# Performance work log

Measured on AMD Instinct MI355X. Metric: run time of the kernel, lower is better.

Reference implementation:

```python
import jax, jax.numpy as jnp
from jax import lax
import numpy as np

RNN = 512; FC = 512; COND = 128; FEAT = 80; NCLS = 256; HALF = RNN // 2
PAD = 2; SCALES = (5, 5, 11); MEL_T = 86  # -> 22550 output samples


def setup_inputs() -> dict:
    key = jax.random.key(0)
    ks = jax.random.split(key, 12)
    s = 0.05
    p = {"mels": jax.random.normal(ks[0], (1, FEAT, MEL_T), jnp.float32)}
    ch = FEAT
    for i, sc in enumerate(SCALES):
        k = 2 * sc + 1
        p[f"up_w{i}"] = jax.random.normal(ks[1 + i], (COND, ch, k), jnp.float32) * s
        p[f"up_b{i}"] = jnp.zeros((COND,), jnp.float32)
        ch = COND
    p["Wx"] = jax.random.normal(ks[4], (3 * RNN, 3 + COND), jnp.float32) * s
    p["bx"] = jnp.zeros((3 * RNN,), jnp.float32)
    p["Wh"] = jax.random.normal(ks[5], (3 * RNN, RNN), jnp.float32) * s
    p["bh"] = jnp.zeros((3 * RNN,), jnp.float32)
    p["O1w"] = jax.random.normal(ks[6], (FC, HALF), jnp.float32) * s
    p["O1b"] = jnp.zeros((FC,), jnp.float32)
    p["O2w"] = jax.random.normal(ks[7], (NCLS, FC), jnp.float32) * s
    p["O2b"] = jnp.zeros((NCLS,), jnp.float32)
    p["O3w"] = jax.random.normal(ks[8], (FC, HALF), jnp.float32) * s
    p["O3b"] = jnp.zeros((FC,), jnp.float32)
    p["O4w"] = jax.random.normal(ks[9], (NCLS, FC), jnp.float32) * s
    p["O4b"] = jnp.zeros((NCLS,), jnp.float32)
    return p


def _upsample(mels, ws, bs):
    # mels[:, :, excess_pad:-excess_pad] with excess_pad = PAD - 1 = 1
    x = mels[:, :, PAD - 1:-(PAD - 1)]
    for w, b, sc in zip(ws, bs, SCALES):
        k = 2 * sc + 1
        # ConvTranspose1d(stride=sc, kernel=k, padding=(3*sc-1)//2) as an
        # input-dilated conv: edge pad = k-1-torch_pad = (sc+1)//2
        e = k - 1 - (3 * sc - 1) // 2
        x = lax.conv_general_dilated(x, w, window_strides=(1,),
                                     padding=[(e, e)], lhs_dilation=(sc,),
                                     dimension_numbers=('NCH', 'OIH', 'NCH'))
        x = jax.nn.relu(x + b[None, :, None])
    return x[0, :, 1:-1].T  # [T, COND]


def _gru(inp, h, Wx, bx, Wh, bh):
    xg = Wx @ inp + bx
    hg = Wh @ h + bh
    xr, xz, xn = jnp.split(xg, 3)
    hr, hz, hn = jnp.split(hg, 3)
    r = jax.nn.sigmoid(xr + hr)
    z = jax.nn.sigmoid(xz + hz)
    n = jnp.tanh(xn + r * hn)
    return (1.0 - z) * n + z * h


def reference(mels, up_w0, up_b0, up_w1, up_b1, up_w2, up_b2,
              Wx, bx, Wh, bh, O1w, O1b, O2w, O2b, O3w, O3b, O4w, O4b):
    cond = _upsample(mels, (up_w0, up_w1, up_w2), (up_b0, up_b1, up_b2))
    zero = jnp.float32(0.0)

    def step(carry, m_t):
        h, c_val, f_val = carry
        # coarse pass: x = [c_{t-1}, f_{t-1}, 0]
        inp1 = jnp.concatenate([jnp.stack([c_val, f_val, zero]), m_t])
        h1 = _gru(inp1, h, Wx, bx, Wh, bh)
        oc = O2w @ jax.nn.relu(O1w @ h1[:HALF] + O1b) + O2b
        c_cat = jnp.argmax(oc).astype(jnp.float32)  # deterministic=True path
        c_new = c_cat / 127.5 - 1.0
        # fine pass: x = [c_{t-1}, f_{t-1}, c_t]
        inp2 = jnp.concatenate([jnp.stack([c_val, f_val, c_new]), m_t])
        h2 = _gru(inp2, h, Wx, bx, Wh, bh)
        of = O4w @ jax.nn.relu(O3w @ h2[HALF:] + O3b) + O4b
        f_cat = jnp.argmax(of).astype(jnp.float32)
        f_new = f_cat / 127.5 - 1.0
        sample = (c_cat * 256.0 + f_cat) / 32767.5 - 1.0
        return (h2, c_new, f_new), (sample, jnp.concatenate([oc, of]))

    init = (jnp.zeros((RNN,), jnp.float32), zero, zero)
    _, (samples, logits) = lax.scan(step, init, cond)
    return samples, logits  # [T], [T, 512]
```

## Files before the change

kernel.cpp:

```cpp
#include <hip/hip_runtime.h>
#include <math.h>

#define T_STEPS 22550
#define NWG 32
#define NTHR 256
#define SLOT 32

#define OF_AM1   64
#define OF_AM2   (OF_AM1 + NWG*SLOT)
#define OF_H1E   (OF_AM2 + NWG*SLOT)
#define OF_O1E   (OF_H1E + 1024)
#define OF_H2E   (OF_O1E + 1024)
#define OF_O3E   (OF_H2E + 1024)
#define OF_BUFA  (OF_O3E + 1024)
#define OF_BUFB  (OF_BUFA + 128*412)
#define OF_COND  (OF_BUFB + 128*2052)

__global__ void k_init(float* ws){
  int i = blockIdx.x*blockDim.x + threadIdx.x;
  ws[OF_AM1 + i] = 0.f;
}

__global__ void k_upconv(const float* __restrict__ x, int instride, int inoff,
                         const float* __restrict__ w, const float* __restrict__ b,
                         float* __restrict__ y, int Cin, int Lin, int K, int sc, int e,
                         int Lout, int mode)
{
  int j = blockIdx.x*blockDim.x + threadIdx.x;
  int c = blockIdx.y;
  if (j >= Lout) return;
  float acc = b[c];
  int kstart = ((e - j) % sc + sc) % sc;
  for (int i = 0; i < Cin; ++i){
    const float* wci = w + (c*Cin + i)*K;
    const float* xi  = x + i*instride + inoff;
    for (int k = kstart; k < K; k += sc){
      int qd = j - e + k;
      if (qd >= 0){
        int qq = qd / sc;
        if (qq < Lin) acc += wci[k]*xi[qq];
      }
    }
  }
  acc = fmaxf(acc, 0.f);
  if (mode == 0) y[c*Lout + j] = acc;
  else { int t = j - 1; if (t >= 0 && t < T_STEPS) y[t*128 + c] = acc; }
}

__device__ __forceinline__ float sigm(float x){ return 1.f/(1.f + expf(-x)); }

typedef unsigned long long ull;

__device__ __forceinline__ void slot_pub(ull* p, float v, unsigned tag){
  ull pk = ((ull)__float_as_uint(v) << 32) | (ull)tag;
  __hip_atomic_store(p, pk, __ATOMIC_RELAXED, __HIP_MEMORY_SCOPE_AGENT);
}
__device__ __forceinline__ float slot_get(ull* p, unsigned tag){
  ull pk;
  for (;;){
    pk = __hip_atomic_load(p, __ATOMIC_RELAXED, __HIP_MEMORY_SCOPE_AGENT);
    if ((unsigned)pk == tag) break;
    __builtin_amdgcn_s_sleep(1);
  }
  return __uint_as_float((unsigned)(pk >> 32));
}

__launch_bounds__(NTHR)
__global__ void k_wavernn(const float* __restrict__ Wx, const float* __restrict__ bx,
                          const float* __restrict__ Wh, const float* __restrict__ bh,
                          const float* __restrict__ O1w, const float* __restrict__ O1b,
                          const float* __restrict__ O2w, const float* __restrict__ O2b,
                          const float* __restrict__ O3w, const float* __restrict__ O3b,
                          const float* __restrict__ O4w, const float* __restrict__ O4b,
                          float* ws, float* __restrict__ out)
{
  __shared__ __align__(16) float smem[1616];
  float* h_s  = smem;
  float* m_s  = smem + 512;
  float* o_s  = smem + 640;
  float* h1c_s= smem + 1152;
  float* hg_s = smem + 1408;
  float* xgb_s= smem + 1456;
  float* xg1_s= smem + 1504;
  float* red_s= smem + 1552;
  float* sc_s = smem + 1560;
  float* wc2_s= smem + 1568;

  const int tid = threadIdx.x, g = blockIdx.x;
  ull* am1 = (ull*)(ws + OF_AM1);
  ull* am2 = (ull*)(ws + OF_AM2);
  ull* h1e = (ull*)(ws + OF_H1E);
  ull* o1e = (ull*)(ws + OF_O1E);
  ull* h2e = (ull*)(ws + OF_H2E);
  ull* o3e = (ull*)(ws + OF_O3E);
  const float* cond = ws + OF_COND;
  float* out_samp = out;
  float* out_log  = out + T_STEPS;

  const int li = tid >> 2, q = tid & 3;
  const int gate = li >> 4, ei = li & 15;
  const int elem = g + 32*ei;
  const int grow = gate*512 + elem;
  float bxv=0.f, bhv=0.f, wc0=0.f, wc1=0.f;
  if (tid < 192 && q == 0){
    bxv = bx[grow]; bhv = bh[grow];
    wc0 = Wx[(size_t)grow*131 + 0]; wc1 = Wx[(size_t)grow*131 + 1];
    wc2_s[li] = Wx[(size_t)grow*131 + 2];
  }

  const int m8 = tid >> 5, l32 = tid & 31, row2 = g + 32*m8;
  float wO2r[16], wO4r[16];
  #pragma unroll
  for (int kk = 0; kk < 16; ++kk){
    wO2r[kk] = O2w[(size_t)row2*512 + l32 + 32*kk];
    wO4r[kk] = O4w[(size_t)row2*512 + l32 + 32*kk];
  }
  const float bO2 = O2b[row2], bO4 = O4b[row2];

  const int m16 = tid >> 4, c16 = tid & 15, rowh = g + 32*m16;
  float wO1r[16], wO3r[16];
  #pragma unroll
  for (int kk = 0; kk < 16; ++kk){
    wO1r[kk] = O1w[(size_t)rowh*256 + c16*16 + kk];
    wO3r[kk] = O3w[(size_t)rowh*256 + c16*16 + kk];
  }
  const float bO1r = O1b[rowh], bO3r = O3b[rowh];

  h_s[tid] = 0.f; h_s[tid+256] = 0.f;
  if (tid < 128) m_s[tid] = cond[tid];
  if (tid == 0){ sc_s[0] = 0.f; sc_s[1] = 0.f; }
  __syncthreads();

  #define COMPUTE_HX() do { \
    if (tid < 192){ \
      const float4* WhR = (const float4*)(Wh + ((size_t)grow*512 + q*128)); \
      const float4* hR  = (const float4*)(h_s + q*128); \
      float aH0 = 0.f, aH1 = 0.f; \
      _Pragma("unroll") \
      for (int kk = 0; kk < 32; kk += 2){ \
        float4 w0 = WhR[kk], v0 = hR[kk]; \
        float4 w1 = WhR[kk+1], v1 = hR[kk+1]; \
        aH0 += w0.x*v0.x + w0.y*v0.y + w0.z*v0.z + w0.w*v0.w; \
        aH1 += w1.x*v1.x + w1.y*v1.y + w1.z*v1.z + w1.w*v1.w; \
      } \
      float accH = aH0 + aH1; \
      const float* WxR = Wx + (size_t)grow*131 + 3 + q*32; \
      const float* mR  = m_s + q*32; \
      float accX = 0.f; \
      _Pragma("unroll") \
      for (int kk = 0; kk < 32; ++kk) accX += WxR[kk]*mR[kk]; \
      accH += __shfl_xor(accH, 1); accH += __shfl_xor(accH, 2); \
      accX += __shfl_xor(accX, 1); accX += __shfl_xor(accX, 2); \
      if (q == 0){ hg_s[li] = accH + bhv; xgb_s[li] = accX + bxv; } \
    } } while(0)

  COMPUTE_HX();

  for (int t = 0; t < T_STEPS; ++t){
    const unsigned tag = (unsigned)(t + 1);
    __syncthreads();

    if (tid < 192 && q == 0) xg1_s[li] = xgb_s[li] + sc_s[0]*wc0 + sc_s[1]*wc1;
    __syncthreads();
    if (tid < 8){
      float r = sigm(xg1_s[tid]      + hg_s[tid]);
      float z = sigm(xg1_s[16+tid]   + hg_s[16+tid]);
      float n = tanhf(xg1_s[32+tid]  + r*hg_s[32+tid]);
      float h1 = (1.f - z)*n + z*h_s[g + 32*tid];
      slot_pub(&h1e[g*16 + tid], h1, tag);
    }
    h1c_s[tid] = slot_get(&h1e[(tid & 31)*16 + (tid >> 5)], tag);
    __syncthreads();

    {
      const float4* hv = (const float4*)(h1c_s + c16*16);
      float acc = 0.f;
      #pragma unroll
      for (int kk = 0; kk < 4; ++kk){
        float4 h4 = hv[kk];
        acc += wO1r[4*kk]*h4.x + wO1r[4*kk+1]*h4.y + wO1r[4*kk+2]*h4.z + wO1r[4*kk+3]*h4.w;
      }
      acc += __shfl_xor(acc, 1); acc += __shfl_xor(acc, 2);
      acc += __shfl_xor(acc, 4); acc += __shfl_xor(acc, 8);
      if (c16 == 0) slot_pub(&o1e[g*16 + m16], fmaxf(acc + bO1r, 0.f), tag);
    }
    {
      int sl = (tid & 31)*16 + (tid >> 5);
      o_s[tid]       = slot_get(&o1e[sl], tag);
      o_s[tid + 256] = slot_get(&o1e[sl + 8], tag);
    }
    __syncthreads();

    {
      float acc = 0.f;
      #pragma unroll
      for (int kk = 0; kk < 16; ++kk) acc += wO2r[kk]*o_s[l32 + 32*kk];
      acc += __shfl_xor(acc, 1); acc += __shfl_xor(acc, 2); acc += __shfl_xor(acc, 4);
      acc += __shfl_xor(acc, 8); acc += __shfl_xor(acc, 16);
      if (l32 == 0){ float v = acc + bO2; out_log[(size_t)t*512 + row2] = v; red_s[m8] = v; }
    }
    __syncthreads();
    if (tid == 0){
      float bv = red_s[0]; int bi = g;
      #pragma unroll
      for (int m = 1; m < 8; ++m){ float v = red_s[m]; if (v > bv){ bv = v; bi = g + 32*m; } }
      ull pk = ((ull)__float_as_uint(bv) << 32) | ((ull)(unsigned)bi << 24) | tag;
      __hip_atomic_store(&am1[g*(SLOT/2)], pk, __ATOMIC_RELAXED, __HIP_MEMORY_SCOPE_AGENT);
    }
    if (tid < 32){
      ull pk;
      for (;;){
        pk = __hip_atomic_load(&am1[tid*(SLOT/2)], __ATOMIC_RELAXED, __HIP_MEMORY_SCOPE_AGENT);
        if ((unsigned)(pk & 0xFFFFFFu) == tag) break;
        __builtin_amdgcn_s_sleep(1);
      }
      float bv = __uint_as_float((unsigned)(pk >> 32));
      int   bi = (int)((pk >> 24) & 0xFFu);
      #pragma unroll
      for (int off = 16; off >= 1; off >>= 1){
        float ov = __shfl_xor(bv, off);
        int   oi = __shfl_xor(bi, off);
        if (ov > bv || (ov == bv && oi < bi)){ bv = ov; bi = oi; }
      }
      if (tid == 0){ sc_s[2] = (float)bi; sc_s[3] = (float)bi/127.5f - 1.f; }
    }
    __syncthreads();

    if (tid < 16){
      float cn = sc_s[3];
      float r = sigm(xg1_s[tid]      + cn*wc2_s[tid]      + hg_s[tid]);
      float z = sigm(xg1_s[16+tid]   + cn*wc2_s[16+tid]   + hg_s[16+tid]);
      float n = tanhf(xg1_s[32+tid]  + cn*wc2_s[32+tid]   + r*hg_s[32+tid]);
      float h2 = (1.f - z)*n + z*h_s[g + 32*tid];
      slot_pub(&h2e[g*16 + tid], h2, tag);
    }
    __syncthreads();
    {
      int sl = (tid & 31)*16 + (tid >> 5);
      h_s[tid]       = slot_get(&h2e[sl], tag);
      h_s[tid + 256] = slot_get(&h2e[sl + 8], tag);
    }
    if (tid < 128 && t + 1 < T_STEPS) m_s[tid] = cond[(size_t)(t+1)*128 + tid];
    __syncthreads();

    {
      const float4* hv = (const float4*)(h_s + 256 + c16*16);
      float acc = 0.f;
      #pragma unroll
      for (int kk = 0; kk < 4; ++kk){
        float4 h4 = hv[kk];
        acc += wO3r[4*kk]*h4.x + wO3r[4*kk+1]*h4.y + wO3r[4*kk+2]*h4.z + wO3r[4*kk+3]*h4.w;
      }
      acc += __shfl_xor(acc, 1); acc += __shfl_xor(acc, 2);
      acc += __shfl_xor(acc, 4); acc += __shfl_xor(acc, 8);
      if (c16 == 0) slot_pub(&o3e[g*16 + m16], fmaxf(acc + bO3r, 0.f), tag);
    }
    {
      int sl = (tid & 31)*16 + (tid >> 5);
      o_s[tid]       = slot_get(&o3e[sl], tag);
      o_s[tid + 256] = slot_get(&o3e[sl + 8], tag);
    }
    __syncthreads();

    {
      float acc = 0.f;
      #pragma unroll
      for (int kk = 0; kk < 16; ++kk) acc += wO4r[kk]*o_s[l32 + 32*kk];
      acc += __shfl_xor(acc, 1); acc += __shfl_xor(acc, 2); acc += __shfl_xor(acc, 4);
      acc += __shfl_xor(acc, 8); acc += __shfl_xor(acc, 16);
      if (l32 == 0){ float v = acc + bO4; out_log[(size_t)t*512 + 256 + row2] = v; red_s[m8] = v; }
    }
    __syncthreads();
    if (tid == 0){
      float bv = red_s[0]; int bi = g;
      #pragma unroll
      for (int m = 1; m < 8; ++m){ float v = red_s[m]; if (v > bv){ bv = v; bi = g + 32*m; } }
      ull pk = ((ull)__float_as_uint(bv) << 32) | ((ull)(unsigned)bi << 24) | tag;
      __hip_atomic_store(&am2[g*(SLOT/2)], pk, __ATOMIC_RELAXED, __HIP_MEMORY_SCOPE_AGENT);
    }

    COMPUTE_HX();

    if (tid < 32){
      ull pk;
      for (;;){
        pk = __hip_atomic_load(&am2[tid*(SLOT/2)], __ATOMIC_RELAXED, __HIP_MEMORY_SCOPE_AGENT);
        if ((unsigned)(pk & 0xFFFFFFu) == tag) break;
        __builtin_amdgcn_s_sleep(1);
      }
      float bv = __uint_as_float((unsigned)(pk >> 32));
      int   bi = (int)((pk >> 24) & 0xFFu);
      #pragma unroll
      for (int off = 16; off >= 1; off >>= 1){
        float ov = __shfl_xor(bv, off);
        int   oi = __shfl_xor(bi, off);
        if (ov > bv || (ov == bv && oi < bi)){ bv = ov; bi = oi; }
      }
      if (tid == 0){
        sc_s[0] = sc_s[3];
        sc_s[1] = (float)bi/127.5f - 1.f;
        if (g == 0) out_samp[t] = (sc_s[2]*256.f + (float)bi)/32767.5f - 1.f;
      }
    }
  }
}

extern "C" void kernel_launch(void* const* d_in, const int* in_sizes, int n_in,
                              void* d_out, int out_size, void* d_ws, size_t ws_size,
                              hipStream_t stream)
{
  const float* mels  = (const float*)d_in[0];
  const float* up_w0 = (const float*)d_in[1]; const float* up_b0 = (const float*)d_in[2];
  const float* up_w1 = (const float*)d_in[3]; const float* up_b1 = (const float*)d_in[4];
  const float* up_w2 = (const float*)d_in[5]; const float* up_b2 = (const float*)d_in[6];
  const float* Wx  = (const float*)d_in[7];  const float* bx  = (const float*)d_in[8];
  const float* Wh  = (const float*)d_in[9];  const float* bh  = (const float*)d_in[10];
  const float* O1w = (const float*)d_in[11]; const float* O1b = (const float*)d_in[12];
  const float* O2w = (const float*)d_in[13]; const float* O2b = (const float*)d_in[14];
  const float* O3w = (const float*)d_in[15]; const float* O3b = (const float*)d_in[16];
  const float* O4w = (const float*)d_in[17]; const float* O4b = (const float*)d_in[18];
  float* ws  = (float*)d_ws;
  float* out = (float*)d_out;

  k_init<<<24, 256, 0, stream>>>(ws);

  k_upconv<<<dim3((412  +127)/128, 128), 128, 0, stream>>>(mels,        86,   1, up_w0, up_b0,
            ws+OF_BUFA,  80,   84, 11,  5, 3,   412, 0);
  k_upconv<<<dim3((2052 +127)/128, 128), 128, 0, stream>>>(ws+OF_BUFA, 412,   0, up_w1, up_b1,
            ws+OF_BUFB, 128,  412, 11,  5, 3,  2052, 0);
  k_upconv<<<dim3((22552+127)/128, 128), 128, 0, stream>>>(ws+OF_BUFB, 2052,  0, up_w2, up_b2,
            ws+OF_COND, 128, 2052, 23, 11, 6, 22552, 1);

  k_wavernn<<<NWG, NTHR, 0, stream>>>(Wx, bx, Wh, bh, O1w, O1b, O2w, O2b,
                                      O3w, O3b, O4w, O4b, ws, out);
}
```

Measured before the change: 339.8 ms.

## Replace O1/O3 exchange rounds with partial-sum publication and redundant argmax

Doubles threads per workgroup to 512. Each workgroup now publishes its partial O2 and O3 products over its own hidden slice, and every workgroup sums all 32 partials itself. This removes one cross-workgroup exchange-and-barrier round for the coarse logits and one for the O3 layer. The coarse argmax is computed redundantly in every workgroup instead of being exchanged through atomics. Spin-waits drop the sleep, and the argmax slots are double-buffered by step parity. In exchange there is more global traffic (32 partials per output), more busy polling, and higher register pressure from the extra per-thread weight caches.

New measurement: 464.0 ms. 1.37x slower.

```diff
diff --git a/kernel.cpp b/kernel.cpp
--- a/kernel.cpp
+++ b/kernel.cpp
@@ -3,22 +3,23 @@
 
 #define T_STEPS 22550
 #define NWG 32
-#define NTHR 256
-#define SLOT 32
-
-#define OF_AM1   64
-#define OF_AM2   (OF_AM1 + NWG*SLOT)
-#define OF_H1E   (OF_AM2 + NWG*SLOT)
-#define OF_O1E   (OF_H1E + 1024)
-#define OF_H2E   (OF_O1E + 1024)
-#define OF_O3E   (OF_H2E + 1024)
-#define OF_BUFA  (OF_O3E + 1024)
+#define NTHR 512
+
+typedef unsigned long long ull;
+
+#define OF_AM2   64
+#define OF_H1E   (OF_AM2 + 2048)
+#define OF_H2E   (OF_H1E + 512)
+#define OF_PLC   (OF_H2E + 1024)
+#define OF_O3P   (OF_PLC + 16384)
+#define OF_SLOTEND (OF_O3P + 32768)
+#define OF_BUFA  OF_SLOTEND
 #define OF_BUFB  (OF_BUFA + 128*412)
 #define OF_COND  (OF_BUFB + 128*2052)
 
 __global__ void k_init(float* ws){
   int i = blockIdx.x*blockDim.x + threadIdx.x;
-  ws[OF_AM1 + i] = 0.f;
+  if (i < (OF_SLOTEND - OF_AM2)) ws[OF_AM2 + i] = 0.f;
 }
 
 __global__ void k_upconv(const float* __restrict__ x, int instride, int inoff,
@@ -49,19 +50,15 @@
 
 __device__ __forceinline__ float sigm(float x){ return 1.f/(1.f + expf(-x)); }
 
-typedef unsigned long long ull;
-
-__device__ __forceinline__ void slot_pub(ull* p, float v, unsigned tag){
-  ull pk = ((ull)__float_as_uint(v) << 32) | (ull)tag;
+__device__ __forceinline__ void pub64(ull* p, ull pk){
   __hip_atomic_store(p, pk, __ATOMIC_RELAXED, __HIP_MEMORY_SCOPE_AGENT);
 }
-__device__ __forceinline__ float slot_get(ull* p, unsigned tag){
-  ull pk;
-  for (;;){
-    pk = __hip_atomic_load(p, __ATOMIC_RELAXED, __HIP_MEMORY_SCOPE_AGENT);
-    if ((unsigned)pk == tag) break;
-    __builtin_amdgcn_s_sleep(1);
-  }
+__device__ __forceinline__ ull ld64(ull* p){
+  return __hip_atomic_load(p, __ATOMIC_RELAXED, __HIP_MEMORY_SCOPE_AGENT);
+}
+__device__ __forceinline__ float spin_get(ull* p, unsigned tag){
+  ull pk = ld64(p);
+  while ((unsigned)pk != tag) pk = ld64(p);
   return __uint_as_float((unsigned)(pk >> 32));
 }
 
@@ -74,84 +71,83 @@
                           const float* __restrict__ O4w, const float* __restrict__ O4b,
                           float* ws, float* __restrict__ out)
 {
-  __shared__ __align__(16) float smem[1616];
-  float* h_s  = smem;
-  float* m_s  = smem + 512;
-  float* o_s  = smem + 640;
-  float* h1c_s= smem + 1152;
-  float* hg_s = smem + 1408;
-  float* xgb_s= smem + 1456;
-  float* xg1_s= smem + 1504;
-  float* red_s= smem + 1552;
-  float* sc_s = smem + 1560;
-  float* wc2_s= smem + 1568;
+  __shared__ __align__(16) float h_s[512];
+  __shared__ __align__(16) float m_s[128];
+  __shared__ __align__(16) float h1c_s[256];
+  __shared__ __align__(16) float o_s[512];
+  __shared__ __align__(16) float logit_s[256];
+  __shared__ float hg_s[48], xgb_s[48], xg1_s[48];
+  __shared__ float o1own_s[16], h2own_s[16];
+  __shared__ float red_s[8], sc_s[8];
+  __shared__ float wc0_s[48], wc1_s[48], wc2_s[48], bx_s[48], bh_s[48];
 
   const int tid = threadIdx.x, g = blockIdx.x;
-  ull* am1 = (ull*)(ws + OF_AM1);
   ull* am2 = (ull*)(ws + OF_AM2);
   ull* h1e = (ull*)(ws + OF_H1E);
-  ull* o1e = (ull*)(ws + OF_O1E);
   ull* h2e = (ull*)(ws + OF_H2E);
-  ull* o3e = (ull*)(ws + OF_O3E);
+  ull* plc = (ull*)(ws + OF_PLC);
+  ull* o3p = (ull*)(ws + OF_O3P);
   const float* cond = ws + OF_COND;
   float* out_samp = out;
   float* out_log  = out + T_STEPS;
 
-  const int li = tid >> 2, q = tid & 3;
-  const int gate = li >> 4, ei = li & 15;
-  const int elem = g + 32*ei;
-  const int grow = gate*512 + elem;
-  float bxv=0.f, bhv=0.f, wc0=0.f, wc1=0.f;
-  if (tid < 192 && q == 0){
-    bxv = bx[grow]; bhv = bh[grow];
-    wc0 = Wx[(size_t)grow*131 + 0]; wc1 = Wx[(size_t)grow*131 + 1];
-    wc2_s[li] = Wx[(size_t)grow*131 + 2];
+  if (tid < 48){
+    int row = (tid>>4)*512 + g + 32*(tid&15);
+    wc0_s[tid] = Wx[(size_t)row*131 + 0];
+    wc1_s[tid] = Wx[(size_t)row*131 + 1];
+    wc2_s[tid] = Wx[(size_t)row*131 + 2];
+    bx_s[tid]  = bx[row];
+    bh_s[tid]  = bh[row];
   }
-
-  const int m8 = tid >> 5, l32 = tid & 31, row2 = g + 32*m8;
-  float wO2r[16], wO4r[16];
+  const int m16 = tid>>5, l32 = tid&31;
+  const int rowO1 = g + 32*m16;
+  float wO1r[8];
   #pragma unroll
-  for (int kk = 0; kk < 16; ++kk){
-    wO2r[kk] = O2w[(size_t)row2*512 + l32 + 32*kk];
-    wO4r[kk] = O4w[(size_t)row2*512 + l32 + 32*kk];
+  for (int k=0;k<8;++k) wO1r[k] = O1w[(size_t)rowO1*256 + l32 + 32*k];
+  const float bO1r = O1b[rowO1];
+  float wPC[16]; float cb2 = 0.f;
+  if (tid < 256){
+    #pragma unroll
+    for (int m=0;m<16;++m) wPC[m] = O2w[(size_t)tid*512 + g + 32*m];
+    cb2 = O2b[tid];
   }
-  const float bO2 = O2b[row2], bO4 = O4b[row2];
-
-  const int m16 = tid >> 4, c16 = tid & 15, rowh = g + 32*m16;
-  float wO1r[16], wO3r[16];
+  float wPF[8];
   #pragma unroll
-  for (int kk = 0; kk < 16; ++kk){
-    wO1r[kk] = O1w[(size_t)rowh*256 + c16*16 + kk];
-    wO3r[kk] = O3w[(size_t)rowh*256 + c16*16 + kk];
-  }
-  const float bO1r = O1b[rowh], bO3r = O3b[rowh];
-
-  h_s[tid] = 0.f; h_s[tid+256] = 0.f;
+  for (int j=0;j<8;++j) wPF[j] = O3w[(size_t)tid*256 + g + 32*j];
+  const float bO3r = O3b[tid];
+  const int mO4 = tid>>6, l64 = tid&63;
+  const int rowO4 = g + 32*mO4;
+  float wO4r[8];
+  #pragma unroll
+  for (int k=0;k<8;++k) wO4r[k] = O4w[(size_t)rowO4*512 + l64 + 64*k];
+  const float bO4r = O4b[rowO4];
+
+  h_s[tid] = 0.f;
   if (tid < 128) m_s[tid] = cond[tid];
   if (tid == 0){ sc_s[0] = 0.f; sc_s[1] = 0.f; }
   __syncthreads();
 
   #define COMPUTE_HX() do { \
-    if (tid < 192){ \
-      const float4* WhR = (const float4*)(Wh + ((size_t)grow*512 + q*128)); \
-      const float4* hR  = (const float4*)(h_s + q*128); \
-      float aH0 = 0.f, aH1 = 0.f; \
+    if (tid < 384){ \
+      const int li_ = tid>>3, p_ = tid&7; \
+      const int row_ = (li_>>4)*512 + g + 32*(li_&15); \
+      const float4* W4 = (const float4*)(Wh + (size_t)row_*512); \
+      const float4* H4 = (const float4*)h_s; \
+      float aH = 0.f; \
       _Pragma("unroll") \
-      for (int kk = 0; kk < 32; kk += 2){ \
-        float4 w0 = WhR[kk], v0 = hR[kk]; \
-        float4 w1 = WhR[kk+1], v1 = hR[kk+1]; \
-        aH0 += w0.x*v0.x + w0.y*v0.y + w0.z*v0.z + w0.w*v0.w; \
-        aH1 += w1.x*v1.x + w1.y*v1.y + w1.z*v1.z + w1.w*v1.w; \
+      for (int kk=0; kk<16; ++kk){ \
+        int f_ = p_*16 + (kk ^ p_); \
+        float4 w = W4[f_], v = H4[f_]; \
+        aH += w.x*v.x + w.y*v.y + w.z*v.z + w.w*v.w; \
       } \
-      float accH = aH0 + aH1; \
-      const float* WxR = Wx + (size_t)grow*131 + 3 + q*32; \
-      const float* mR  = m_s + q*32; \
-      float accX = 0.f; \
+      const float* WxR = Wx + (size_t)row_*131 + 3 + p_*16; \
+      const float* mR  = m_s + p_*16; \
+      float aX = 0.f; \
       _Pragma("unroll") \
-      for (int kk = 0; kk < 32; ++kk) accX += WxR[kk]*mR[kk]; \
-      accH += __shfl_xor(accH, 1); accH += __shfl_xor(accH, 2); \
-      accX += __shfl_xor(accX, 1); accX += __shfl_xor(accX, 2); \
-      if (q == 0){ hg_s[li] = accH + bhv; xgb_s[li] = accX + bxv; } \
+      for (int kk=0; kk<16; ++kk) aX += WxR[kk]*mR[kk]; \
+      aH += __shfl_xor(aH,1); aH += __shfl_xor(aH,2); aH += __shfl_xor(aH,4); \
+      aX += __shfl_xor(aX,1); aX += __shfl_xor(aX,2); aX += __shfl_xor(aX,4); \
+      if (p_ == 0){ hg_s[li_] = aH + bh_s[li_]; xgb_s[li_] = aX + bx_s[li_]; } \
     } } while(0)
 
   COMPUTE_HX();
@@ -160,140 +156,128 @@
     const unsigned tag = (unsigned)(t + 1);
     __syncthreads();
 
-    if (tid < 192 && q == 0) xg1_s[li] = xgb_s[li] + sc_s[0]*wc0 + sc_s[1]*wc1;
-    __syncthreads();
+    if (tid < 48) xg1_s[tid] = xgb_s[tid] + sc_s[0]*wc0_s[tid] + sc_s[1]*wc1_s[tid];
+    __syncthreads();
+
     if (tid < 8){
-      float r = sigm(xg1_s[tid]      + hg_s[tid]);
-      float z = sigm(xg1_s[16+tid]   + hg_s[16+tid]);
-      float n = tanhf(xg1_s[32+tid]  + r*hg_s[32+tid]);
+      float r = sigm(xg1_s[tid]     + hg_s[tid]);
+      float z = sigm(xg1_s[16+tid]  + hg_s[16+tid]);
+      float n = tanhf(xg1_s[32+tid] + r*hg_s[32+tid]);
       float h1 = (1.f - z)*n + z*h_s[g + 32*tid];
-      slot_pub(&h1e[g*16 + tid], h1, tag);
-    }
-    h1c_s[tid] = slot_get(&h1e[(tid & 31)*16 + (tid >> 5)], tag);
-    __syncthreads();
-
-    {
-      const float4* hv = (const float4*)(h1c_s + c16*16);
-      float acc = 0.f;
-      #pragma unroll
-      for (int kk = 0; kk < 4; ++kk){
-        float4 h4 = hv[kk];
-        acc += wO1r[4*kk]*h4.x + wO1r[4*kk+1]*h4.y + wO1r[4*kk+2]*h4.z + wO1r[4*kk+3]*h4.w;
-      }
-      acc += __shfl_xor(acc, 1); acc += __shfl_xor(acc, 2);
-      acc += __shfl_xor(acc, 4); acc += __shfl_xor(acc, 8);
-      if (c16 == 0) slot_pub(&o1e[g*16 + m16], fmaxf(acc + bO1r, 0.f), tag);
-    }
-    {
-      int sl = (tid & 31)*16 + (tid >> 5);
-      o_s[tid]       = slot_get(&o1e[sl], tag);
-      o_s[tid + 256] = slot_get(&o1e[sl + 8], tag);
-    }
+      pub64(&h1e[g*8 + tid], ((ull)__float_as_uint(h1) << 32) | tag);
+    }
+    if (tid < 256) h1c_s[tid] = spin_get(&h1e[(tid & 31)*8 + (tid >> 5)], tag);
     __syncthreads();
 
     {
       float acc = 0.f;
       #pragma unroll
-      for (int kk = 0; kk < 16; ++kk) acc += wO2r[kk]*o_s[l32 + 32*kk];
-      acc += __shfl_xor(acc, 1); acc += __shfl_xor(acc, 2); acc += __shfl_xor(acc, 4);
-      acc += __shfl_xor(acc, 8); acc += __shfl_xor(acc, 16);
-      if (l32 == 0){ float v = acc + bO2; out_log[(size_t)t*512 + row2] = v; red_s[m8] = v; }
+      for (int k=0;k<8;++k) acc += wO1r[k]*h1c_s[l32 + 32*k];
+      acc += __shfl_xor(acc,1); acc += __shfl_xor(acc,2); acc += __shfl_xor(acc,4);
+      acc += __shfl_xor(acc,8); acc += __shfl_xor(acc,16);
+      if (l32 == 0) o1own_s[m16] = fmaxf(acc + bO1r, 0.f);
+    }
+    __syncthreads();
+
+    if (tid < 256){
+      float s = 0.f;
+      #pragma unroll
+      for (int m=0;m<16;++m) s += wPC[m]*o1own_s[m];
+      pub64(&plc[g*256 + tid], ((ull)__float_as_uint(s) << 32) | tag);
+    }
+    if (tid < 256){
+      ull v[32];
+      #pragma unroll
+      for (int g2=0; g2<32; ++g2) v[g2] = ld64(&plc[g2*256 + tid]);
+      float s = cb2;
+      #pragma unroll
+      for (int g2=0; g2<32; ++g2){
+        ull pk = v[g2];
+        while ((unsigned)pk != tag) pk = ld64(&plc[g2*256 + tid]);
+        s += __uint_as_float((unsigned)(pk >> 32));
+      }
+      logit_s[tid] = s;
+    }
+    __syncthreads();
+    if (tid < 8) out_log[(size_t)t*512 + 8*g + tid] = logit_s[8*g + tid];
+    if (tid < 64){
+      float bv = logit_s[tid]; int bi = tid;
+      #pragma unroll
+      for (int j=1;j<4;++j){ float v2 = logit_s[tid + 64*j]; if (v2 > bv){ bv = v2; bi = tid + 64*j; } }
+      #pragma unroll
+      for (int off=32; off>=1; off>>=1){
+        float ov = __shfl_xor(bv,off); int oi = __shfl_xor(bi,off);
+        if (ov > bv || (ov == bv && oi < bi)){ bv = ov; bi = oi; }
+      }
+      if (tid == 0){ sc_s[2] = (float)bi; sc_s[3] = (float)bi/127.5f - 1.f; }
+    }
+    __syncthreads();
+
+    if (tid < 16){
+      float cn = sc_s[3];
+      float r = sigm(xg1_s[tid]     + cn*wc2_s[tid]     + hg_s[tid]);
+      float z = sigm(xg1_s[16+tid]  + cn*wc2_s[16+tid]  + hg_s[16+tid]);
+      float n = tanhf(xg1_s[32+tid] + cn*wc2_s[32+tid]  + r*hg_s[32+tid]);
+      float h2 = (1.f - z)*n + z*h_s[g + 32*tid];
+      h2own_s[tid] = h2;
+      pub64(&h2e[g*16 + tid], ((ull)__float_as_uint(h2) << 32) | tag);
+    }
+    __syncthreads();
+    {
+      float s = 0.f;
+      #pragma unroll
+      for (int j=0;j<8;++j) s += wPF[j]*h2own_s[8 + j];
+      pub64(&o3p[g*512 + tid], ((ull)__float_as_uint(s) << 32) | tag);
+    }
+    h_s[tid] = spin_get(&h2e[(tid & 31)*16 + (tid >> 5)], tag);
+    if (tid < 128 && t + 1 < T_STEPS) m_s[tid] = cond[(size_t)(t+1)*128 + tid];
+    {
+      ull v[32];
+      #pragma unroll
+      for (int g2=0; g2<32; ++g2) v[g2] = ld64(&o3p[g2*512 + tid]);
+      float s = bO3r;
+      #pragma unroll
+      for (int g2=0; g2<32; ++g2){
+        ull pk = v[g2];
+        while ((unsigned)pk != tag) pk = ld64(&o3p[g2*512 + tid]);
+        s += __uint_as_float((unsigned)(pk >> 32));
+      }
+      o_s[tid] = fmaxf(s, 0.f);
+    }
+    __syncthreads();
+
+    {
+      float acc = 0.f;
+      #pragma unroll
+      for (int k=0;k<8;++k) acc += wO4r[k]*o_s[l64 + 64*k];
+      acc += __shfl_xor(acc,1); acc += __shfl_xor(acc,2); acc += __shfl_xor(acc,4);
+      acc += __shfl_xor(acc,8); acc += __shfl_xor(acc,16); acc += __shfl_xor(acc,32);
+      if (l64 == 0){
+        float v = acc + bO4r;
+        out_log[(size_t)t*512 + 256 + rowO4] = v;
+        red_s[mO4] = v;
+      }
     }
     __syncthreads();
     if (tid == 0){
       float bv = red_s[0]; int bi = g;
       #pragma unroll
-      for (int m = 1; m < 8; ++m){ float v = red_s[m]; if (v > bv){ bv = v; bi = g + 32*m; } }
-      ull pk = ((ull)__float_as_uint(bv) << 32) | ((ull)(unsigned)bi << 24) | tag;
-      __hip_atomic_store(&am1[g*(SLOT/2)], pk, __ATOMIC_RELAXED, __HIP_MEMORY_SCOPE_AGENT);
-    }
+      for (int m=1;m<8;++m){ float v = red_s[m]; if (v > bv){ bv = v; bi = g + 32*m; } }
+      pub64(&am2[((t & 1)*NWG + g)*16],
+            ((ull)__float_as_uint(bv) << 32) | ((ull)(unsigned)bi << 24) | tag);
+    }
+
+    COMPUTE_HX();
+
     if (tid < 32){
-      ull pk;
-      for (;;){
-        pk = __hip_atomic_load(&am1[tid*(SLOT/2)], __ATOMIC_RELAXED, __HIP_MEMORY_SCOPE_AGENT);
-        if ((unsigned)(pk & 0xFFFFFFu) == tag) break;
-        __builtin_amdgcn_s_sleep(1);
-      }
+      ull* sl = &am2[((t & 1)*NWG + tid)*16];
+      ull pk = ld64(sl);
+      while ((unsigned)(pk & 0xFFFFFFu) != tag) pk = ld64(sl);
       float bv = __uint_as_float((unsigned)(pk >> 32));
       int   bi = (int)((pk >> 24) & 0xFFu);
       #pragma unroll
-      for (int off = 16; off >= 1; off >>= 1){
-        float ov = __shfl_xor(bv, off);
-        int   oi = __shfl_xor(bi, off);
-        if (ov > bv || (ov == bv && oi < bi)){ bv = ov; bi = oi; }
-      }
-      if (tid == 0){ sc_s[2] = (float)bi; sc_s[3] = (float)bi/127.5f - 1.f; }
-    }
-    __syncthreads();
-
-    if (tid < 16){
-      float cn = sc_s[3];
-      float r = sigm(xg1_s[tid]      + cn*wc2_s[tid]      + hg_s[tid]);
-      float z = sigm(xg1_s[16+tid]   + cn*wc2_s[16+tid]   + hg_s[16+tid]);
-      float n = tanhf(xg1_s[32+tid]  + cn*wc2_s[32+tid]   + r*hg_s[32+tid]);
-      float h2 = (1.f - z)*n + z*h_s[g + 32*tid];
-      slot_pub(&h2e[g*16 + tid], h2, tag);
-    }
-    __syncthreads();
-    {
-      int sl = (tid & 31)*16 + (tid >> 5);
-      h_s[tid]       = slot_get(&h2e[sl], tag);
-      h_s[tid + 256] = slot_get(&h2e[sl + 8], tag);
-    }
-    if (tid < 128 && t + 1 < T_STEPS) m_s[tid] = cond[(size_t)(t+1)*128 + tid];
-    __syncthreads();
-
-    {
-      const float4* hv = (const float4*)(h_s + 256 + c16*16);
-      float acc = 0.f;
-      #pragma unroll
-      for (int kk = 0; kk < 4; ++kk){
-        float4 h4 = hv[kk];
-        acc += wO3r[4*kk]*h4.x + wO3r[4*kk+1]*h4.y + wO3r[4*kk+2]*h4.z + wO3r[4*kk+3]*h4.w;
-      }
-      acc += __shfl_xor(acc, 1); acc += __shfl_xor(acc, 2);
-      acc += __shfl_xor(acc, 4); acc += __shfl_xor(acc, 8);
-      if (c16 == 0) slot_pub(&o3e[g*16 + m16], fmaxf(acc + bO3r, 0.f), tag);
-    }
-    {
-      int sl = (tid & 31)*16 + (tid >> 5);
-      o_s[tid]       = slot_get(&o3e[sl], tag);
-      o_s[tid + 256] = slot_get(&o3e[sl + 8], tag);
-    }
-    __syncthreads();
-
-    {
-      float acc = 0.f;
-      #pragma unroll
-      for (int kk = 0; kk < 16; ++kk) acc += wO4r[kk]*o_s[l32 + 32*kk];
-      acc += __shfl_xor(acc, 1); acc += __shfl_xor(acc, 2); acc += __shfl_xor(acc, 4);
-      acc += __shfl_xor(acc, 8); acc += __shfl_xor(acc, 16);
-      if (l32 == 0){ float v = acc + bO4; out_log[(size_t)t*512 + 256 + row2] = v; red_s[m8] = v; }
-    }
-    __syncthreads();
-    if (tid == 0){
-      float bv = red_s[0]; int bi = g;
-      #pragma unroll
-      for (int m = 1; m < 8; ++m){ float v = red_s[m]; if (v > bv){ bv = v; bi = g + 32*m; } }
-      ull pk = ((ull)__float_as_uint(bv) << 32) | ((ull)(unsigned)bi << 24) | tag;
-      __hip_atomic_store(&am2[g*(SLOT/2)], pk, __ATOMIC_RELAXED, __HIP_MEMORY_SCOPE_AGENT);
-    }
-
-    COMPUTE_HX();
-
-    if (tid < 32){
-      ull pk;
-      for (;;){
-        pk = __hip_atomic_load(&am2[tid*(SLOT/2)], __ATOMIC_RELAXED, __HIP_MEMORY_SCOPE_AGENT);
-        if ((unsigned)(pk & 0xFFFFFFu) == tag) break;
-        __builtin_amdgcn_s_sleep(1);
-      }
-      float bv = __uint_as_float((unsigned)(pk >> 32));
-      int   bi = (int)((pk >> 24) & 0xFFu);
-      #pragma unroll
-      for (int off = 16; off >= 1; off >>= 1){
-        float ov = __shfl_xor(bv, off);
-        int   oi = __shfl_xor(bi, off);
+      for (int off=16; off>=1; off>>=1){
+        float ov = __shfl_xor(bv,off); int oi = __shfl_xor(bi,off);
         if (ov > bv || (ov == bv && oi < bi)){ bv = ov; bi = oi; }
       }
       if (tid == 0){
@@ -322,7 +306,7 @@
   float* ws  = (float*)d_ws;
   float* out = (float*)d_out;
 
-  k_init<<<24, 256, 0, stream>>>(ws);
+  k_init<<<((OF_SLOTEND-OF_AM2) + 255)/256, 256, 0, stream>>>(ws);
 
   k_upconv<<<dim3((412  +127)/128, 128), 128, 0, stream>>>(mels,        86,   1, up_w0, up_b0,
             ws+OF_BUFA,  80,   84, 11,  5, 3,   412, 0);
```
